# Kernel optimization log

Measured on AMD Instinct MI355X. Metric: run time of the kernel, lower is better.

The kernel has to match this reference:

```python
import jax, jax.numpy as jnp
import numpy as np

BS, H, L, D = 16, 16, 4096, 32  # bs, n_heads, seq_len(=q_len), head_dim

def setup_inputs() -> dict:
    key = jax.random.key(0)
    kq, kk, kv = jax.random.split(key, 3)
    q = jax.random.normal(kq, (BS, H, L, D), dtype=jnp.float32)
    k = jax.random.normal(kk, (BS, H, D, L), dtype=jnp.float32)
    v = jax.random.normal(kv, (BS, H, L, D), dtype=jnp.float32)
    return {"q": q, "k": k, "v": v}

def reference(q, k, v):
    # reordered attention: scores = (k @ v) / sqrt(seq_len) -> [bs,h,d_k,d_v]
    seq_len = v.shape[2]
    scores = jnp.einsum('bhds,bhse->bhde', k, v) / jnp.sqrt(jnp.float32(seq_len))
    # faithful to source: softmax over dim=0 (the batch dimension)
    attn_weights = jax.nn.softmax(scores, axis=0)
    # dropout p=0.0 -> identity
    # output = q @ weights -> [bs,h,q_len,d_v]
    output = jnp.einsum('bhld,bhde->bhle', q, attn_weights)
    return output, attn_weights
```

## Files before the change

### kernel.cpp

```cpp
#include <hip/hip_runtime.h>

#define BS 16
#define NH 16
#define LQ 4096
#define DH 32

constexpr size_t OUT_ELEMS = (size_t)BS * NH * LQ * DH;
constexpr int HDE = NH * DH * DH;

__device__ __forceinline__ void async_cp16(float* dst, const float* src) {
    __builtin_amdgcn_global_load_lds(
        (const __attribute__((address_space(1))) void*)src,
        (__attribute__((address_space(3))) void*)dst, 16, 0, 0);
}

__device__ __forceinline__ void fma4(float4& a, float s, const float4& v) {
    a.x = fmaf(s, v.x, a.x);
    a.y = fmaf(s, v.y, a.y);
    a.z = fmaf(s, v.z, a.z);
    a.w = fmaf(s, v.w, a.w);
}

template<int NCH>
__global__ __launch_bounds__(256, 5) void kv_partial(const float* __restrict__ k,
                                                     const float* __restrict__ v,
                                                     float* __restrict__ part) {
    __shared__ float lds[8192];
    const int tid  = threadIdx.x;
    const int wid  = tid >> 6;
    const int lane = tid & 63;
    const int nsplit = 32 / NCH;
    const int p  = blockIdx.x % nsplit;
    const int bh = blockIdx.x / nsplit;

    const int dgl = lane >> 3;
    const int d0  = dgl << 2;
    const int e0  = (lane & 7) << 2;

    const float* kb = k + (size_t)bh * DH * LQ;
    const float* vb = v + (size_t)bh * LQ * DH;
    float* kt = lds;
    float* vt = lds + 4096;

    size_t ksrc[4];
    int kdst[4];
    size_t vsrc[4];
#pragma unroll
    for (int i = 0; i < 4; ++i) {
        const int j = (wid << 2) + i;
        const int d = (j << 1) + (lane >> 5);
        const int gs = lane & 31;
        const int gsrc = (gs & 24) | ((gs ^ ((j >> 1) & 7)) & 7);
        ksrc[i] = (size_t)d * LQ + (gsrc << 2);
        kdst[i] = j << 8;
        vsrc[i] = (size_t)(j << 8) + (lane << 2);
    }

    float4 acc0 = {0,0,0,0}, acc1 = {0,0,0,0}, acc2 = {0,0,0,0}, acc3 = {0,0,0,0};

#pragma unroll
    for (int c = 0; c < NCH; ++c) {
        const int s0 = (p * NCH + c) << 7;
#pragma unroll
        for (int i = 0; i < 4; ++i) async_cp16(kt + kdst[i], kb + ksrc[i] + s0);
#pragma unroll
        for (int i = 0; i < 4; ++i) async_cp16(vt + kdst[i], vb + ((size_t)s0 << 5) + vsrc[i]);
        __syncthreads();

#pragma unroll
        for (int gg = 0; gg < 8; ++gg) {
            const int g  = (wid << 3) + gg;
            const int ko = ((g & 24) | ((g ^ dgl) & 7)) << 2;
            const float4 kq0 = *(const float4*)(kt + ((d0 + 0) << 7) + ko);
            const float4 kq1 = *(const float4*)(kt + ((d0 + 1) << 7) + ko);
            const float4 kq2 = *(const float4*)(kt + ((d0 + 2) << 7) + ko);
            const float4 kq3 = *(const float4*)(kt + ((d0 + 3) << 7) + ko);
            const int vo = (g << 7) + e0;
            const float4 vv0 = *(const float4*)(vt + vo);
            const float4 vv1 = *(const float4*)(vt + vo + 32);
            const float4 vv2 = *(const float4*)(vt + vo + 64);
            const float4 vv3 = *(const float4*)(vt + vo + 96);

            fma4(acc0, kq0.x, vv0); fma4(acc0, kq0.y, vv1); fma4(acc0, kq0.z, vv2); fma4(acc0, kq0.w, vv3);
            fma4(acc1, kq1.x, vv0); fma4(acc1, kq1.y, vv1); fma4(acc1, kq1.z, vv2); fma4(acc1, kq1.w, vv3);
            fma4(acc2, kq2.x, vv0); fma4(acc2, kq2.y, vv1); fma4(acc2, kq2.z, vv2); fma4(acc2, kq2.w, vv3);
            fma4(acc3, kq3.x, vv0); fma4(acc3, kq3.y, vv1); fma4(acc3, kq3.z, vv2); fma4(acc3, kq3.w, vv3);
        }
        __syncthreads();
    }

    *(float4*)(lds + (wid << 10) + ((d0 + 0) << 5) + e0) = acc0;
    *(float4*)(lds + (wid << 10) + ((d0 + 1) << 5) + e0) = acc1;
    *(float4*)(lds + (wid << 10) + ((d0 + 2) << 5) + e0) = acc2;
    *(float4*)(lds + (wid << 10) + ((d0 + 3) << 5) + e0) = acc3;
    __syncthreads();

    const int t4 = tid << 2;
    const float4 r0 = *(const float4*)(lds + t4);
    const float4 r1 = *(const float4*)(lds + 1024 + t4);
    const float4 r2 = *(const float4*)(lds + 2048 + t4);
    const float4 r3 = *(const float4*)(lds + 3072 + t4);
    float4 r;
    r.x = (r0.x + r1.x) + (r2.x + r3.x);
    r.y = (r0.y + r1.y) + (r2.y + r3.y);
    r.z = (r0.z + r1.z) + (r2.z + r3.z);
    r.w = (r0.w + r1.w) + (r2.w + r3.w);
    *(float4*)(part + ((size_t)p * (BS * NH) + bh) * 1024 + t4) = r;
}

__global__ __launch_bounds__(256) void reduce_p(const float* __restrict__ part,
                                                float* __restrict__ scores, int nsp) {
    const int gidx = blockIdx.x * 256 + threadIdx.x;
    const int b    = gidx >> 14;
    const int idx  = gidx & 16383;
    float s = 0.f;
    for (int pp = 0; pp < nsp; ++pp)
        s += part[((size_t)pp << 18) + ((size_t)b << 14) + idx];
    scores[gidx] = s * (1.0f / 64.0f);
}

__global__ __launch_bounds__(256) void softmax_b(float* __restrict__ wts) {
    const int idx = blockIdx.x * 256 + threadIdx.x;

    float sc[BS];
#pragma unroll
    for (int b = 0; b < BS; ++b) sc[b] = wts[((size_t)b << 14) + idx];
    float m = sc[0];
#pragma unroll
    for (int b = 1; b < BS; ++b) m = fmaxf(m, sc[b]);
    float sum = 0.f;
#pragma unroll
    for (int b = 0; b < BS; ++b) { sc[b] = __expf(sc[b] - m); sum += sc[b]; }
    float inv = 1.0f / sum;
#pragma unroll
    for (int b = 0; b < BS; ++b) wts[((size_t)b << 14) + idx] = sc[b] * inv;
}

__global__ __launch_bounds__(256, 2) void qw(const float* __restrict__ q,
                                             const float* __restrict__ wts,
                                             float* __restrict__ out) {
    __shared__ float qs[128 * 36];
    const int blk = blockIdx.x;
    const int bh  = blk >> 5;
    const int lt  = blk & 31;
    const int tid = threadIdx.x;

    const float* qbase = q + ((size_t)bh * LQ + lt * 128) * DH;

#pragma unroll
    for (int pp = 0; pp < 4; ++pp) {
        const int idx = pp * 256 + tid;
        const int row = idx >> 3;
        const int c4  = idx & 7;
        const float4 t = *(const float4*)(qbase + idx * 4);
        *(float4*)(qs + row * 36 + c4 * 4) = t;
    }

    const int lsub = tid >> 3;
    const int e0   = (tid & 7) << 2;

    const int b = bh >> 4, h = bh & 15;
    float4 Wf[32];
    const float* wbase = wts + ((size_t)b << 14) + ((size_t)h << 10) + e0;
#pragma unroll
    for (int d = 0; d < 32; ++d) Wf[d] = *(const float4*)(wbase + d * DH);

    __syncthreads();

    float* obase = out + ((size_t)bh * LQ + lt * 128) * DH;

#pragma unroll
    for (int r = 0; r < 4; ++r) {
        const int lr = lsub + r * 32;
        const float* qrow = qs + lr * 36;
        float4 acc = {0,0,0,0};
#pragma unroll
        for (int d4 = 0; d4 < 32; d4 += 4) {
            const float4 qv = *(const float4*)(qrow + d4);
            fma4(acc, qv.x, Wf[d4 + 0]);
            fma4(acc, qv.y, Wf[d4 + 1]);
            fma4(acc, qv.z, Wf[d4 + 2]);
            fma4(acc, qv.w, Wf[d4 + 3]);
        }
        *(float4*)(obase + (size_t)lr * DH + e0) = acc;
    }
}

extern "C" void kernel_launch(void* const* d_in, const int* in_sizes, int n_in,
                              void* d_out, int out_size, void* d_ws, size_t ws_size,
                              hipStream_t stream) {
    const float* q = (const float*)d_in[0];
    const float* k = (const float*)d_in[1];
    const float* v = (const float*)d_in[2];
    float* out  = (float*)d_out;
    float* wts  = out + OUT_ELEMS;
    float* part = (float*)d_ws;

    const size_t need32 = (size_t)32 * 256 * 1024 * 4;
    int nsp;
    if (ws_size >= need32) {
        kv_partial<1><<<256 * 32, 256, 0, stream>>>(k, v, part);
        nsp = 32;
    } else {
        kv_partial<4><<<256 * 8, 256, 0, stream>>>(k, v, part);
        nsp = 8;
    }
    reduce_p<<<(BS * HDE) / 256, 256, 0, stream>>>(part, wts, nsp);
    softmax_b<<<HDE / 256, 256, 0, stream>>>(wts);
    qw<<<BS * NH * (LQ / 128), 256, 0, stream>>>(q, wts, out);
}
```

Before: 146.0 us.

## Restructure kv_partial register tiling and fuse split reduction into softmax

The kv_partial kernel now loads V straight from global memory into registers instead of staging it in LDS. Each thread computes an 8x4 output tile over a quarter of the sequence chunk, and the two half-waves are combined with xor shuffles before a padded LDS reduction. The separate reduce_p and softmax_b kernels are merged into one finalize_w kernel, which removes a launch and a round trip of the scores through global memory. The trade-offs are more registers per thread (launch bounds lowered to 3) and a finalize kernel with fewer threads, each doing the split-sum for all 16 batches.

```diff
diff --git a/kernel.cpp b/kernel.cpp
--- a/kernel.cpp
+++ b/kernel.cpp
@@ -22,116 +22,131 @@
 }
 
 template<int NCH>
-__global__ __launch_bounds__(256, 5) void kv_partial(const float* __restrict__ k,
+__global__ __launch_bounds__(256, 3) void kv_partial(const float* __restrict__ k,
                                                      const float* __restrict__ v,
                                                      float* __restrict__ part) {
-    __shared__ float lds[8192];
-    const int tid  = threadIdx.x;
-    const int wid  = tid >> 6;
-    const int lane = tid & 63;
+    __shared__ float lds[4608];
+    const int tid = threadIdx.x;
+    const int w   = tid >> 6;
+    const int l   = tid & 63;
     const int nsplit = 32 / NCH;
     const int p  = blockIdx.x % nsplit;
     const int bh = blockIdx.x / nsplit;
 
-    const int dgl = lane >> 3;
-    const int d0  = dgl << 2;
-    const int e0  = (lane & 7) << 2;
+    const int tw = tid & 31;
+    const int sp = tid >> 5;
+    const int dg = tw >> 3;
+    const int eg = tw & 7;
+    const int d0 = dg << 3;
+    const int e0 = eg << 2;
 
     const float* kb = k + (size_t)bh * DH * LQ;
     const float* vb = v + (size_t)bh * LQ * DH;
-    float* kt = lds;
-    float* vt = lds + 4096;
 
     size_t ksrc[4];
-    int kdst[4];
-    size_t vsrc[4];
-#pragma unroll
-    for (int i = 0; i < 4; ++i) {
-        const int j = (wid << 2) + i;
-        const int d = (j << 1) + (lane >> 5);
-        const int gs = lane & 31;
-        const int gsrc = (gs & 24) | ((gs ^ ((j >> 1) & 7)) & 7);
-        ksrc[i] = (size_t)d * LQ + (gsrc << 2);
-        kdst[i] = j << 8;
-        vsrc[i] = (size_t)(j << 8) + (lane << 2);
-    }
-
-    float4 acc0 = {0,0,0,0}, acc1 = {0,0,0,0}, acc2 = {0,0,0,0}, acc3 = {0,0,0,0};
+#pragma unroll
+    for (int jj = 0; jj < 4; ++jj) {
+        const int j = (w << 2) | jj;
+        const int d = (j << 1) + (l >> 5);
+        const int csrc = (l & 31) ^ ((j >> 2) & 3);
+        ksrc[jj] = (size_t)d * LQ + (csrc << 2);
+    }
+
+    float4 acc[8];
+#pragma unroll
+    for (int i = 0; i < 8; ++i) acc[i] = make_float4(0.f, 0.f, 0.f, 0.f);
 
 #pragma unroll
     for (int c = 0; c < NCH; ++c) {
         const int s0 = (p * NCH + c) << 7;
-#pragma unroll
-        for (int i = 0; i < 4; ++i) async_cp16(kt + kdst[i], kb + ksrc[i] + s0);
-#pragma unroll
-        for (int i = 0; i < 4; ++i) async_cp16(vt + kdst[i], vb + ((size_t)s0 << 5) + vsrc[i]);
+        if (c > 0) __syncthreads();
+
+#pragma unroll
+        for (int jj = 0; jj < 4; ++jj)
+            async_cp16(lds + (((w << 2) | jj) << 8), kb + ksrc[jj] + s0);
+
+        float4 vv[4][4];
+        const float* vbase = vb + ((size_t)(s0 + (sp << 4)) << 5) + e0;
+#pragma unroll
+        for (int st = 0; st < 4; ++st)
+#pragma unroll
+            for (int u = 0; u < 4; ++u)
+                vv[st][u] = *(const float4*)(vbase + ((st << 2) + u) * DH);
+
         __syncthreads();
 
 #pragma unroll
-        for (int gg = 0; gg < 8; ++gg) {
-            const int g  = (wid << 3) + gg;
-            const int ko = ((g & 24) | ((g ^ dgl) & 7)) << 2;
-            const float4 kq0 = *(const float4*)(kt + ((d0 + 0) << 7) + ko);
-            const float4 kq1 = *(const float4*)(kt + ((d0 + 1) << 7) + ko);
-            const float4 kq2 = *(const float4*)(kt + ((d0 + 2) << 7) + ko);
-            const float4 kq3 = *(const float4*)(kt + ((d0 + 3) << 7) + ko);
-            const int vo = (g << 7) + e0;
-            const float4 vv0 = *(const float4*)(vt + vo);
-            const float4 vv1 = *(const float4*)(vt + vo + 32);
-            const float4 vv2 = *(const float4*)(vt + vo + 64);
-            const float4 vv3 = *(const float4*)(vt + vo + 96);
-
-            fma4(acc0, kq0.x, vv0); fma4(acc0, kq0.y, vv1); fma4(acc0, kq0.z, vv2); fma4(acc0, kq0.w, vv3);
-            fma4(acc1, kq1.x, vv0); fma4(acc1, kq1.y, vv1); fma4(acc1, kq1.z, vv2); fma4(acc1, kq1.w, vv3);
-            fma4(acc2, kq2.x, vv0); fma4(acc2, kq2.y, vv1); fma4(acc2, kq2.z, vv2); fma4(acc2, kq2.w, vv3);
-            fma4(acc3, kq3.x, vv0); fma4(acc3, kq3.y, vv1); fma4(acc3, kq3.z, vv2); fma4(acc3, kq3.w, vv3);
+        for (int st = 0; st < 4; ++st) {
+            const int ko = (((sp << 2) + st) ^ dg) << 2;
+            float4 kq[8];
+#pragma unroll
+            for (int i = 0; i < 8; ++i)
+                kq[i] = *(const float4*)(lds + ((d0 + i) << 7) + ko);
+#pragma unroll
+            for (int u = 0; u < 4; ++u) {
+                const float4 vu = vv[st][u];
+#pragma unroll
+                for (int i = 0; i < 8; ++i) {
+                    const float ks = (u == 0) ? kq[i].x
+                                   : (u == 1) ? kq[i].y
+                                   : (u == 2) ? kq[i].z : kq[i].w;
+                    fma4(acc[i], ks, vu);
+                }
+            }
         }
-        __syncthreads();
-    }
-
-    *(float4*)(lds + (wid << 10) + ((d0 + 0) << 5) + e0) = acc0;
-    *(float4*)(lds + (wid << 10) + ((d0 + 1) << 5) + e0) = acc1;
-    *(float4*)(lds + (wid << 10) + ((d0 + 2) << 5) + e0) = acc2;
-    *(float4*)(lds + (wid << 10) + ((d0 + 3) << 5) + e0) = acc3;
+    }
+
+#pragma unroll
+    for (int i = 0; i < 8; ++i) {
+        acc[i].x += __shfl_xor(acc[i].x, 32);
+        acc[i].y += __shfl_xor(acc[i].y, 32);
+        acc[i].z += __shfl_xor(acc[i].z, 32);
+        acc[i].w += __shfl_xor(acc[i].w, 32);
+    }
+
     __syncthreads();
-
-    const int t4 = tid << 2;
-    const float4 r0 = *(const float4*)(lds + t4);
-    const float4 r1 = *(const float4*)(lds + 1024 + t4);
-    const float4 r2 = *(const float4*)(lds + 2048 + t4);
-    const float4 r3 = *(const float4*)(lds + 3072 + t4);
-    float4 r;
-    r.x = (r0.x + r1.x) + (r2.x + r3.x);
-    r.y = (r0.y + r1.y) + (r2.y + r3.y);
-    r.z = (r0.z + r1.z) + (r2.z + r3.z);
-    r.w = (r0.w + r1.w) + (r2.w + r3.w);
-    *(float4*)(part + ((size_t)p * (BS * NH) + bh) * 1024 + t4) = r;
-}
-
-__global__ __launch_bounds__(256) void reduce_p(const float* __restrict__ part,
-                                                float* __restrict__ scores, int nsp) {
-    const int gidx = blockIdx.x * 256 + threadIdx.x;
-    const int b    = gidx >> 14;
-    const int idx  = gidx & 16383;
-    float s = 0.f;
-    for (int pp = 0; pp < nsp; ++pp)
-        s += part[((size_t)pp << 18) + ((size_t)b << 14) + idx];
-    scores[gidx] = s * (1.0f / 64.0f);
-}
-
-__global__ __launch_bounds__(256) void softmax_b(float* __restrict__ wts) {
+    if (l < 32) {
+        float* dst = lds + w * 1152 + l * 36;
+#pragma unroll
+        for (int i = 0; i < 8; ++i) *(float4*)(dst + (i << 2)) = acc[i];
+    }
+    __syncthreads();
+
+    const int fdg = (tid >> 6) & 3;
+    const int fi  = (tid >> 3) & 7;
+    const int feg = tid & 7;
+    const int off = (fdg * 8 + feg) * 36 + (fi << 2);
+    float4 r0 = *(const float4*)(lds + off);
+    const float4 r1 = *(const float4*)(lds + 1152 + off);
+    const float4 r2 = *(const float4*)(lds + 2304 + off);
+    const float4 r3 = *(const float4*)(lds + 3456 + off);
+    r0.x = (r0.x + r1.x) + (r2.x + r3.x);
+    r0.y = (r0.y + r1.y) + (r2.y + r3.y);
+    r0.z = (r0.z + r1.z) + (r2.z + r3.z);
+    r0.w = (r0.w + r1.w) + (r2.w + r3.w);
+    *(float4*)(part + ((size_t)p * (BS * NH) + bh) * 1024 + (tid << 2)) = r0;
+}
+
+__global__ __launch_bounds__(256) void finalize_w(const float* __restrict__ part,
+                                                  float* __restrict__ wts, int nsp) {
     const int idx = blockIdx.x * 256 + threadIdx.x;
 
     float sc[BS];
 #pragma unroll
-    for (int b = 0; b < BS; ++b) sc[b] = wts[((size_t)b << 14) + idx];
+    for (int b = 0; b < BS; ++b) {
+        float s = 0.f;
+        for (int pp = 0; pp < nsp; ++pp)
+            s += part[((size_t)pp << 18) + ((size_t)b << 14) + idx];
+        sc[b] = s * (1.0f / 64.0f);
+    }
+
     float m = sc[0];
 #pragma unroll
     for (int b = 1; b < BS; ++b) m = fmaxf(m, sc[b]);
     float sum = 0.f;
 #pragma unroll
     for (int b = 0; b < BS; ++b) { sc[b] = __expf(sc[b] - m); sum += sc[b]; }
-    float inv = 1.0f / sum;
+    const float inv = 1.0f / sum;
 #pragma unroll
     for (int b = 0; b < BS; ++b) wts[((size_t)b << 14) + idx] = sc[b] * inv;
 }
@@ -173,7 +188,7 @@
     for (int r = 0; r < 4; ++r) {
         const int lr = lsub + r * 32;
         const float* qrow = qs + lr * 36;
-        float4 acc = {0,0,0,0};
+        float4 acc = {0, 0, 0, 0};
 #pragma unroll
         for (int d4 = 0; d4 < 32; d4 += 4) {
             const float4 qv = *(const float4*)(qrow + d4);
@@ -205,7 +220,6 @@
         kv_partial<4><<<256 * 8, 256, 0, stream>>>(k, v, part);
         nsp = 8;
     }
-    reduce_p<<<(BS * HDE) / 256, 256, 0, stream>>>(part, wts, nsp);
-    softmax_b<<<HDE / 256, 256, 0, stream>>>(wts);
+    finalize_w<<<HDE / 256, 256, 0, stream>>>(part, wts, nsp);
     qw<<<BS * NH * (LQ / 128), 256, 0, stream>>>(q, wts, out);
 }
```

Measured after the change: 243.5 us. 1.67x slower.
